# Optimization experiments

Hardware: AMD Instinct MI355X
Metric: run time of the kernel (lower is better)

Reference implementation:

```python
import jax, jax.numpy as jnp
import numpy as np
import math

H = 768      # hidden_dim
NH = 12      # nhead
HD = H // NH # head_dim
FF = 4 * H
B, N = 8, 1024


def _layernorm(x, g, b, eps=1e-5):
    m = jnp.mean(x, axis=-1, keepdims=True)
    v = jnp.var(x, axis=-1, keepdims=True)
    return (x - m) * jax.lax.rsqrt(v + eps) * g + b


def setup_inputs() -> dict:
    key = jax.random.key(0)
    ks = jax.random.split(key, 16)
    s = 1.0 / math.sqrt(H)
    inp = {
        'x': jax.random.normal(ks[0], (B, N, H), jnp.float32),
        'attn_bias': jax.random.normal(ks[1], (NH, N, N), jnp.float32),
        'Wq': jax.random.normal(ks[2], (H, H), jnp.float32) * s,
        'bq': jnp.zeros((H,), jnp.float32),
        'Wk': jax.random.normal(ks[3], (H, H), jnp.float32) * s,
        'bk': jnp.zeros((H,), jnp.float32),
        'Wv': jax.random.normal(ks[4], (H, H), jnp.float32) * s,
        'bv': jnp.zeros((H,), jnp.float32),
        'Wo': jax.random.normal(ks[5], (H, H), jnp.float32) * s,
        'bo': jnp.zeros((H,), jnp.float32),
        'g1': jnp.ones((H,), jnp.float32),
        'be1': jnp.zeros((H,), jnp.float32),
        'W1': jax.random.normal(ks[6], (H, FF), jnp.float32) * s,
        'bf1': jnp.zeros((FF,), jnp.float32),
        'W2': jax.random.normal(ks[7], (FF, H), jnp.float32) * (1.0 / math.sqrt(FF)),
        'bf2': jnp.zeros((H,), jnp.float32),
        'g2': jnp.ones((H,), jnp.float32),
        'be2': jnp.zeros((H,), jnp.float32),
    }
    return inp


def reference(x, attn_bias, Wq, bq, Wk, bk, Wv, bv, Wo, bo, g1, be1, W1, bf1, W2, bf2, g2, be2):
    # dropout in eval mode (identity)
    Bc, Nc, C = x.shape
    q = (x @ Wq + bq).reshape(Bc, Nc, NH, HD).transpose(0, 2, 1, 3)  # [B,H,N,D]
    k = (x @ Wk + bk).reshape(Bc, Nc, NH, HD).transpose(0, 2, 1, 3)
    v = (x @ Wv + bv).reshape(Bc, Nc, NH, HD).transpose(0, 2, 1, 3)
    scores = jnp.einsum('bhnd,bhmd->bhnm', q, k) / math.sqrt(HD)
    scores = scores + attn_bias[None]  # bias broadcast over batch
    probs = jax.nn.softmax(scores, axis=-1)
    out = jnp.einsum('bhnm,bhmd->bhnd', probs, v)
    out = out.transpose(0, 2, 1, 3).reshape(Bc, Nc, C)
    out = out @ Wo + bo
    x = _layernorm(x + out, g1, be1)
    h = jax.nn.gelu(x @ W1 + bf1, approximate=False) @ W2 + bf2
    x = _layernorm(x + h, g2, be2)
    return x
```

## Files before the change

### kernel.cpp

```cpp
#include <hip/hip_runtime.h>
#include <math.h>

#define NH 12
#define HD 64
#define SEQ 1024
#define BATCH 8
#define HDIM 768
#define FFDIM 3072
#define MTOT (BATCH*SEQ)

typedef __attribute__((ext_vector_type(8))) short short8;
typedef __attribute__((ext_vector_type(4))) float f32x4;
typedef __attribute__((ext_vector_type(4))) unsigned short ushort4v;

__device__ __forceinline__ unsigned short f2b(float f) {
    union { float f; unsigned u; } v; v.f = f;
    unsigned r = v.u + 0x7fffu + ((v.u >> 16) & 1u);
    return (unsigned short)(r >> 16);
}

__device__ __forceinline__ f32x4 mfma16(short8 a, short8 b, f32x4 c) {
    return __builtin_amdgcn_mfma_f32_16x16x32_bf16(a, b, c, 0, 0, 0);
}

__global__ __launch_bounds__(256) void k_cvt(const float* __restrict__ in,
                                             unsigned short* __restrict__ out, int n) {
    int idx = (blockIdx.x * 256 + threadIdx.x) * 4;
    if (idx >= n) return;
    float4 v = *reinterpret_cast<const float4*>(in + idx);
    ushort4v o;
    o[0] = f2b(v.x); o[1] = f2b(v.y); o[2] = f2b(v.z); o[3] = f2b(v.w);
    *reinterpret_cast<ushort4v*>(out + idx) = o;
}

__global__ __launch_bounds__(256) void k_wt(const float* __restrict__ W,
                                            unsigned short* __restrict__ WT, int K, int Nn) {
    __shared__ float t[32][33];
    int n0 = blockIdx.x * 32, k0 = blockIdx.y * 32;
    int x = threadIdx.x, y = threadIdx.y;
#pragma unroll
    for (int i = y; i < 32; i += 8) t[i][x] = W[(size_t)(k0 + i) * Nn + n0 + x];
    __syncthreads();
#pragma unroll
    for (int i = y; i < 32; i += 8) WT[(size_t)(n0 + i) * K + k0 + x] = f2b(t[x][i]);
}

__global__ void k_bias3(const float* __restrict__ a, const float* __restrict__ b,
                        const float* __restrict__ c, float* __restrict__ o) {
    int i = blockIdx.x * 256 + threadIdx.x;
    if (i >= 3 * HDIM) return;
    o[i] = (i < HDIM) ? a[i] : (i < 2 * HDIM ? b[i - HDIM] : c[i - 2 * HDIM]);
}

template<int EPI>
__global__ __launch_bounds__(256) void k_gemm(const unsigned short* __restrict__ A,
                                              const unsigned short* __restrict__ BT,
                                              const float* __restrict__ bias,
                                              const float* __restrict__ resid,
                                              unsigned short* __restrict__ outb,
                                              float* __restrict__ outf,
                                              int Mdim, int Ndim, int Kdim) {
    __shared__ unsigned short As[128][40];
    __shared__ unsigned short Bs[128][40];
    int tid = threadIdx.x;
    int wid = tid >> 6, lane = tid & 63;
    int wm = wid >> 1, wn = wid & 1;
    int l15 = lane & 15, l16 = lane >> 4;
    int bm = blockIdx.x * 128, bn = blockIdx.y * 128;

    f32x4 acc[4][4] = {};

    for (int kt = 0; kt < Kdim; kt += 32) {
#pragma unroll
        for (int it = 0; it < 2; ++it) {
            int idx = tid + it * 256;
            int r = idx >> 2, c8 = (idx & 3) * 8;
            *reinterpret_cast<short8*>(&As[r][c8]) =
                *reinterpret_cast<const short8*>(&A[(size_t)(bm + r) * Kdim + kt + c8]);
            *reinterpret_cast<short8*>(&Bs[r][c8]) =
                *reinterpret_cast<const short8*>(&BT[(size_t)(bn + r) * Kdim + kt + c8]);
        }
        __syncthreads();
        short8 af[4], bfr[4];
#pragma unroll
        for (int i = 0; i < 4; i++)
            af[i] = *reinterpret_cast<const short8*>(&As[wm * 64 + i * 16 + l15][l16 * 8]);
#pragma unroll
        for (int i = 0; i < 4; i++)
            bfr[i] = *reinterpret_cast<const short8*>(&Bs[wn * 64 + i * 16 + l15][l16 * 8]);
#pragma unroll
        for (int i = 0; i < 4; i++)
#pragma unroll
            for (int j = 0; j < 4; j++)
                acc[i][j] = mfma16(af[i], bfr[j], acc[i][j]);
        __syncthreads();
    }

#pragma unroll
    for (int i = 0; i < 4; i++) {
#pragma unroll
        for (int j = 0; j < 4; j++) {
            int grow0 = bm + wm * 64 + i * 16 + l16 * 4;
            int gcol = bn + wn * 64 + j * 16 + l15;
            float bcol = bias[gcol];
#pragma unroll
            for (int r = 0; r < 4; r++) {
                int grow = grow0 + r;
                float v = acc[i][j][r] + bcol;
                size_t oi = (size_t)grow * Ndim + gcol;
                if constexpr (EPI == 0) {
                    outb[oi] = f2b(v);
                } else if constexpr (EPI == 1) {
                    outf[oi] = v + resid[oi];
                } else {
                    float g = 0.5f * v * (1.0f + erff(v * 0.70710678118654752f));
                    outb[oi] = f2b(g);
                }
            }
        }
    }
}

__global__ __launch_bounds__(256) void k_attn(const unsigned short* __restrict__ QKV,
                                              const float* __restrict__ bias,
                                              unsigned short* __restrict__ out) {
    __shared__ unsigned short Ks[64][72];
    __shared__ unsigned short Vt[64][72];
    __shared__ unsigned short Ps[4][16][72];

    int bh = blockIdx.y;
    int b = bh / NH, h = bh % NH;
    int q0 = blockIdx.x * 64;
    int tid = threadIdx.x, wid = tid >> 6, lane = tid & 63;
    int l15 = lane & 15, l16 = lane >> 4;

    size_t qrow = (size_t)(b * SEQ + q0 + wid * 16 + l15) * 2304 + h * 64;
    short8 qf0 = *reinterpret_cast<const short8*>(&QKV[qrow + l16 * 8]);
    short8 qf1 = *reinterpret_cast<const short8*>(&QKV[qrow + 32 + l16 * 8]);

    f32x4 o[4] = {};
    float mrow[4], lrow[4];
#pragma unroll
    for (int r = 0; r < 4; r++) { mrow[r] = -1e30f; lrow[r] = 0.0f; }

    for (int kt = 0; kt < SEQ; kt += 64) {
#pragma unroll
        for (int it = 0; it < 2; ++it) {
            int idx = tid + it * 256;
            int r = idx >> 3, c8 = (idx & 7) * 8;
            size_t gr = (size_t)(b * SEQ + kt + r) * 2304 + h * 64;
            *reinterpret_cast<short8*>(&Ks[r][c8]) =
                *reinterpret_cast<const short8*>(&QKV[gr + 768 + c8]);
            short8 vv = *reinterpret_cast<const short8*>(&QKV[gr + 1536 + c8]);
            int cc = r ^ c8;
#pragma unroll
            for (int j = 0; j < 8; j++) Vt[c8 + j][cc] = (unsigned short)vv[j];
        }
        __syncthreads();

        f32x4 s[4];
#pragma unroll
        for (int c = 0; c < 4; c++) {
            f32x4 t = {};
            t = mfma16(qf0, *reinterpret_cast<const short8*>(&Ks[c * 16 + l15][l16 * 8]), t);
            t = mfma16(qf1, *reinterpret_cast<const short8*>(&Ks[c * 16 + l15][32 + l16 * 8]), t);
            s[c] = t;
        }
#pragma unroll
        for (int c = 0; c < 4; c++)
#pragma unroll
            for (int r = 0; r < 4; r++) {
                size_t bi = (size_t)h * SEQ * SEQ +
                            (size_t)(q0 + wid * 16 + l16 * 4 + r) * SEQ + kt + c * 16 + l15;
                s[c][r] = s[c][r] * 0.125f + bias[bi];
            }
#pragma unroll
        for (int r = 0; r < 4; r++) {
            float mx = fmaxf(fmaxf(s[0][r], s[1][r]), fmaxf(s[2][r], s[3][r]));
#pragma unroll
            for (int off = 1; off < 16; off <<= 1) mx = fmaxf(mx, __shfl_xor(mx, off, 64));
            float mnew = fmaxf(mrow[r], mx);
            float resc = __expf(mrow[r] - mnew);
            mrow[r] = mnew;
            float sum = 0.0f;
#pragma unroll
            for (int c = 0; c < 4; c++) {
                float p = __expf(s[c][r] - mnew);
                s[c][r] = p; sum += p;
            }
#pragma unroll
            for (int off = 1; off < 16; off <<= 1) sum += __shfl_xor(sum, off, 64);
            lrow[r] = lrow[r] * resc + sum;
#pragma unroll
            for (int dc = 0; dc < 4; dc++) o[dc][r] *= resc;
        }
#pragma unroll
        for (int c = 0; c < 4; c++)
#pragma unroll
            for (int r = 0; r < 4; r++)
                Ps[wid][l16 * 4 + r][c * 16 + l15] = f2b(s[c][r]);
#pragma unroll
        for (int dc = 0; dc < 4; dc++) {
            int d = dc * 16 + l15;
            int sw = ((d >> 3) & 7) << 3;
#pragma unroll
            for (int kk = 0; kk < 2; kk++) {
                short8 pa = *reinterpret_cast<const short8*>(&Ps[wid][l15][kk * 32 + l16 * 8]);
                short8 vb = *reinterpret_cast<const short8*>(&Vt[d][(kk * 32 + l16 * 8) ^ sw]);
                o[dc] = mfma16(pa, vb, o[dc]);
            }
        }
        __syncthreads();
    }

#pragma unroll
    for (int dc = 0; dc < 4; dc++)
#pragma unroll
        for (int r = 0; r < 4; r++) {
            float v = o[dc][r] / lrow[r];
            size_t row = (size_t)(b * SEQ + q0 + wid * 16 + l16 * 4 + r);
            out[row * 768 + h * 64 + dc * 16 + l15] = f2b(v);
        }
}

template<int WB>
__global__ __launch_bounds__(256) void k_ln(const float* __restrict__ in,
                                            const float* __restrict__ gw,
                                            const float* __restrict__ bw,
                                            float* __restrict__ outf,
                                            unsigned short* __restrict__ outb) {
    int row = blockIdx.x, tid = threadIdx.x;
    const float* x = in + (size_t)row * 768;
    float v0 = x[tid], v1 = x[tid + 256], v2 = x[tid + 512];
    float s = v0 + v1 + v2;
    float s2 = v0 * v0 + v1 * v1 + v2 * v2;
#pragma unroll
    for (int off = 32; off; off >>= 1) {
        s += __shfl_down(s, off, 64);
        s2 += __shfl_down(s2, off, 64);
    }
    __shared__ float red[16];
    if ((tid & 63) == 0) { red[tid >> 6] = s; red[8 + (tid >> 6)] = s2; }
    __syncthreads();
    float ssum = red[0] + red[1] + red[2] + red[3];
    float s2sum = red[8] + red[9] + red[10] + red[11];
    float mean = ssum * (1.0f / 768.0f);
    float var = s2sum * (1.0f / 768.0f) - mean * mean;
    float rstd = rsqrtf(var + 1e-5f);
    float* of = outf + (size_t)row * 768;
    unsigned short* ob = outb ? outb + (size_t)row * 768 : nullptr;
    float vv[3] = { v0, v1, v2 };
#pragma unroll
    for (int i = 0; i < 3; i++) {
        int col = tid + i * 256;
        float y = (vv[i] - mean) * rstd * gw[col] + bw[col];
        of[col] = y;
        if constexpr (WB) ob[col] = f2b(y);
    }
}

constexpr size_t OFF_XB    = 0;
constexpr size_t OFF_QKV   = OFF_XB    + 12582912;
constexpr size_t OFF_ATT   = OFF_QKV   + 37748736;
constexpr size_t OFF_WQKVT = OFF_ATT   + 12582912;
constexpr size_t OFF_WOT   = OFF_WQKVT + 3538944;
constexpr size_t OFF_W1T   = OFF_WOT   + 1179648;
constexpr size_t OFF_W2T   = OFF_W1T   + 4718592;
constexpr size_t OFF_BQKV  = OFF_W2T   + 4718592;
constexpr size_t OFF_TMP   = OFF_BQKV  + 9216;
constexpr size_t OFF_X1F   = OFF_TMP   + 25165824;
constexpr size_t OFF_X1B   = OFF_X1F   + 25165824;
constexpr size_t OFF_H     = OFF_X1B   + 12582912;

extern "C" void kernel_launch(void* const* d_in, const int* in_sizes, int n_in,
                              void* d_out, int out_size, void* d_ws, size_t ws_size,
                              hipStream_t stream) {
    const float* x    = (const float*)d_in[0];
    const float* ab   = (const float*)d_in[1];
    const float* Wq   = (const float*)d_in[2];
    const float* bq   = (const float*)d_in[3];
    const float* Wk   = (const float*)d_in[4];
    const float* bk   = (const float*)d_in[5];
    const float* Wv   = (const float*)d_in[6];
    const float* bv   = (const float*)d_in[7];
    const float* Wo   = (const float*)d_in[8];
    const float* bo   = (const float*)d_in[9];
    const float* g1   = (const float*)d_in[10];
    const float* be1  = (const float*)d_in[11];
    const float* W1   = (const float*)d_in[12];
    const float* bf1  = (const float*)d_in[13];
    const float* W2   = (const float*)d_in[14];
    const float* bf2  = (const float*)d_in[15];
    const float* g2   = (const float*)d_in[16];
    const float* be2  = (const float*)d_in[17];

    char* ws = (char*)d_ws;
    unsigned short* xb    = (unsigned short*)(ws + OFF_XB);
    unsigned short* qkv   = (unsigned short*)(ws + OFF_QKV);
    unsigned short* att   = (unsigned short*)(ws + OFF_ATT);
    unsigned short* wqkvt = (unsigned short*)(ws + OFF_WQKVT);
    unsigned short* wot   = (unsigned short*)(ws + OFF_WOT);
    unsigned short* w1t   = (unsigned short*)(ws + OFF_W1T);
    unsigned short* w2t   = (unsigned short*)(ws + OFF_W2T);
    float*          bqkv  = (float*)(ws + OFF_BQKV);
    float*          tmp   = (float*)(ws + OFF_TMP);
    float*          x1f   = (float*)(ws + OFF_X1F);
    unsigned short* x1b   = (unsigned short*)(ws + OFF_X1B);
    unsigned short* hb    = (unsigned short*)(ws + OFF_H);
    float*          out   = (float*)d_out;

    k_cvt<<<dim3(MTOT * HDIM / 1024), dim3(256), 0, stream>>>(x, xb, MTOT * HDIM);
    k_wt<<<dim3(24, 24), dim3(32, 8), 0, stream>>>(Wq, wqkvt, HDIM, HDIM);
    k_wt<<<dim3(24, 24), dim3(32, 8), 0, stream>>>(Wk, wqkvt + 768 * 768, HDIM, HDIM);
    k_wt<<<dim3(24, 24), dim3(32, 8), 0, stream>>>(Wv, wqkvt + 2 * 768 * 768, HDIM, HDIM);
    k_wt<<<dim3(24, 24), dim3(32, 8), 0, stream>>>(Wo, wot, HDIM, HDIM);
    k_wt<<<dim3(96, 24), dim3(32, 8), 0, stream>>>(W1, w1t, HDIM, FFDIM);
    k_wt<<<dim3(24, 96), dim3(32, 8), 0, stream>>>(W2, w2t, FFDIM, HDIM);
    k_bias3<<<dim3(9), dim3(256), 0, stream>>>(bq, bk, bv, bqkv);

    k_gemm<0><<<dim3(64, 18), dim3(256), 0, stream>>>(xb, wqkvt, bqkv, nullptr, qkv, nullptr,
                                                      MTOT, 3 * HDIM, HDIM);
    k_attn<<<dim3(SEQ / 64, BATCH * NH), dim3(256), 0, stream>>>(qkv, ab, att);
    k_gemm<1><<<dim3(64, 6), dim3(256), 0, stream>>>(att, wot, bo, x, nullptr, tmp,
                                                     MTOT, HDIM, HDIM);
    k_ln<1><<<dim3(MTOT), dim3(256), 0, stream>>>(tmp, g1, be1, x1f, x1b);
    k_gemm<2><<<dim3(64, 24), dim3(256), 0, stream>>>(x1b, w1t, bf1, nullptr, hb, nullptr,
                                                      MTOT, FFDIM, HDIM);
    k_gemm<1><<<dim3(64, 6), dim3(256), 0, stream>>>(hb, w2t, bf2, x1f, nullptr, tmp,
                                                     MTOT, FFDIM == FFDIM ? HDIM : HDIM, FFDIM);
    k_ln<0><<<dim3(MTOT), dim3(256), 0, stream>>>(tmp, g2, be2, out, nullptr);
}
```

Before: 514.3 us.

## Use direct global-to-LDS async loads with XOR swizzle and K-tile 64 in GEMM

The GEMM mainloop now copies A and B tiles straight from global memory into LDS with global_load_lds instead of staging them through registers. The K tile grows from 32 to 64, and an XOR swizzle on columns replaces the padded layout to avoid LDS bank conflicts. The Q/K/V/O weight transposes are merged into one 3D-grid launch, which assumes the Wo buffer sits directly after the QKV weights in the workspace. Tiles are still single-buffered and synchronised with barriers, so global-load latency is not overlapped with MFMA work.

Measured after the change: 496.2 us. -3.5%, faster.

```diff
diff --git a/kernel.cpp b/kernel.cpp
--- a/kernel.cpp
+++ b/kernel.cpp
@@ -21,6 +21,12 @@
 
 __device__ __forceinline__ f32x4 mfma16(short8 a, short8 b, f32x4 c) {
     return __builtin_amdgcn_mfma_f32_16x16x32_bf16(a, b, c, 0, 0, 0);
+}
+
+__device__ __forceinline__ void async_copy16(const unsigned short* g, unsigned short* l) {
+    __builtin_amdgcn_global_load_lds(
+        (const __attribute__((address_space(1))) unsigned int*)(const void*)g,
+        (__attribute__((address_space(3))) unsigned int*)(void*)l, 16, 0, 0);
 }
 
 __global__ __launch_bounds__(256) void k_cvt(const float* __restrict__ in,
@@ -33,11 +39,29 @@
     *reinterpret_cast<ushort4v*>(out + idx) = o;
 }
 
+__global__ __launch_bounds__(256) void k_wt4(const float* __restrict__ W0,
+                                             const float* __restrict__ W1,
+                                             const float* __restrict__ W2,
+                                             const float* __restrict__ W3,
+                                             unsigned short* __restrict__ WT) {
+    __shared__ float t[32][33];
+    const float* W = (blockIdx.z == 0) ? W0 : (blockIdx.z == 1) ? W1 :
+                     (blockIdx.z == 2) ? W2 : W3;
+    unsigned short* dst = WT + (size_t)blockIdx.z * 768 * 768;
+    int n0 = blockIdx.x * 32, k0 = blockIdx.y * 32;
+    int x = threadIdx.x & 31, y = threadIdx.x >> 5;
+#pragma unroll
+    for (int i = y; i < 32; i += 8) t[i][x] = W[(size_t)(k0 + i) * 768 + n0 + x];
+    __syncthreads();
+#pragma unroll
+    for (int i = y; i < 32; i += 8) dst[(size_t)(n0 + i) * 768 + k0 + x] = f2b(t[x][i]);
+}
+
 __global__ __launch_bounds__(256) void k_wt(const float* __restrict__ W,
                                             unsigned short* __restrict__ WT, int K, int Nn) {
     __shared__ float t[32][33];
     int n0 = blockIdx.x * 32, k0 = blockIdx.y * 32;
-    int x = threadIdx.x, y = threadIdx.y;
+    int x = threadIdx.x & 31, y = threadIdx.x >> 5;
 #pragma unroll
     for (int i = y; i < 32; i += 8) t[i][x] = W[(size_t)(k0 + i) * Nn + n0 + x];
     __syncthreads();
@@ -60,39 +84,47 @@
                                               unsigned short* __restrict__ outb,
                                               float* __restrict__ outf,
                                               int Mdim, int Ndim, int Kdim) {
-    __shared__ unsigned short As[128][40];
-    __shared__ unsigned short Bs[128][40];
+    __shared__ unsigned short As[128 * 64];
+    __shared__ unsigned short Bs[128 * 64];
     int tid = threadIdx.x;
     int wid = tid >> 6, lane = tid & 63;
     int wm = wid >> 1, wn = wid & 1;
     int l15 = lane & 15, l16 = lane >> 4;
     int bm = blockIdx.x * 128, bn = blockIdx.y * 128;
 
+    int srow = wid * 8 + (lane >> 3);
+    int scol = 8 * ((lane & 7) ^ (lane >> 3));
+    const unsigned short* aptr = A + (size_t)(bm + srow) * Kdim + scol;
+    const unsigned short* bptr = BT + (size_t)(bn + srow) * Kdim + scol;
+
     f32x4 acc[4][4] = {};
-
-    for (int kt = 0; kt < Kdim; kt += 32) {
-#pragma unroll
-        for (int it = 0; it < 2; ++it) {
-            int idx = tid + it * 256;
-            int r = idx >> 2, c8 = (idx & 3) * 8;
-            *reinterpret_cast<short8*>(&As[r][c8]) =
-                *reinterpret_cast<const short8*>(&A[(size_t)(bm + r) * Kdim + kt + c8]);
-            *reinterpret_cast<short8*>(&Bs[r][c8]) =
-                *reinterpret_cast<const short8*>(&BT[(size_t)(bn + r) * Kdim + kt + c8]);
+    const int swz = (l15 & 7) << 3;
+
+    for (int kt = 0; kt < Kdim; kt += 64) {
+#pragma unroll
+        for (int c = 0; c < 4; c++) {
+            async_copy16(aptr + (size_t)c * 32 * Kdim + kt, As + c * 2048 + wid * 512);
+            async_copy16(bptr + (size_t)c * 32 * Kdim + kt, Bs + c * 2048 + wid * 512);
         }
         __syncthreads();
-        short8 af[4], bfr[4];
-#pragma unroll
-        for (int i = 0; i < 4; i++)
-            af[i] = *reinterpret_cast<const short8*>(&As[wm * 64 + i * 16 + l15][l16 * 8]);
-#pragma unroll
-        for (int i = 0; i < 4; i++)
-            bfr[i] = *reinterpret_cast<const short8*>(&Bs[wn * 64 + i * 16 + l15][l16 * 8]);
-#pragma unroll
-        for (int i = 0; i < 4; i++)
-#pragma unroll
-            for (int j = 0; j < 4; j++)
-                acc[i][j] = mfma16(af[i], bfr[j], acc[i][j]);
+        short8 af[2][4], bfr[2][4];
+#pragma unroll
+        for (int kk = 0; kk < 2; kk++)
+#pragma unroll
+            for (int i = 0; i < 4; i++) {
+                int ra = wm * 64 + i * 16 + l15;
+                int rb = wn * 64 + i * 16 + l15;
+                int cidx = (kk * 32 + l16 * 8) ^ swz;
+                af[kk][i]  = *reinterpret_cast<const short8*>(&As[ra * 64 + cidx]);
+                bfr[kk][i] = *reinterpret_cast<const short8*>(&Bs[rb * 64 + cidx]);
+            }
+#pragma unroll
+        for (int kk = 0; kk < 2; kk++)
+#pragma unroll
+            for (int i = 0; i < 4; i++)
+#pragma unroll
+                for (int j = 0; j < 4; j++)
+                    acc[i][j] = mfma16(af[kk][i], bfr[kk][j], acc[i][j]);
         __syncthreads();
     }
 
@@ -310,12 +342,9 @@
     float*          out   = (float*)d_out;
 
     k_cvt<<<dim3(MTOT * HDIM / 1024), dim3(256), 0, stream>>>(x, xb, MTOT * HDIM);
-    k_wt<<<dim3(24, 24), dim3(32, 8), 0, stream>>>(Wq, wqkvt, HDIM, HDIM);
-    k_wt<<<dim3(24, 24), dim3(32, 8), 0, stream>>>(Wk, wqkvt + 768 * 768, HDIM, HDIM);
-    k_wt<<<dim3(24, 24), dim3(32, 8), 0, stream>>>(Wv, wqkvt + 2 * 768 * 768, HDIM, HDIM);
-    k_wt<<<dim3(24, 24), dim3(32, 8), 0, stream>>>(Wo, wot, HDIM, HDIM);
-    k_wt<<<dim3(96, 24), dim3(32, 8), 0, stream>>>(W1, w1t, HDIM, FFDIM);
-    k_wt<<<dim3(24, 96), dim3(32, 8), 0, stream>>>(W2, w2t, FFDIM, HDIM);
+    k_wt4<<<dim3(24, 24, 4), dim3(256), 0, stream>>>(Wq, Wk, Wv, Wo, wqkvt);
+    k_wt<<<dim3(96, 24), dim3(256), 0, stream>>>(W1, w1t, HDIM, FFDIM);
+    k_wt<<<dim3(24, 96), dim3(256), 0, stream>>>(W2, w2t, FFDIM, HDIM);
     k_bias3<<<dim3(9), dim3(256), 0, stream>>>(bq, bk, bv, bqkv);
 
     k_gemm<0><<<dim3(64, 18), dim3(256), 0, stream>>>(xb, wqkvt, bqkv, nullptr, qkv, nullptr,
@@ -327,6 +356,6 @@
     k_gemm<2><<<dim3(64, 24), dim3(256), 0, stream>>>(x1b, w1t, bf1, nullptr, hb, nullptr,
                                                       MTOT, FFDIM, HDIM);
     k_gemm<1><<<dim3(64, 6), dim3(256), 0, stream>>>(hb, w2t, bf2, x1f, nullptr, tmp,
-                                                     MTOT, FFDIM == FFDIM ? HDIM : HDIM, FFDIM);
+                                                     MTOT, HDIM, FFDIM);
     k_ln<0><<<dim3(MTOT), dim3(256), 0, stream>>>(tmp, g2, be2, out, nullptr);
 }
```
